# Kernel optimization log

Hardware: AMD Instinct MI355X
Metric: run time of the kernel (lower is better)

Reference implementation:

```python
import jax, jax.numpy as jnp
import numpy as np

B, S, N, F, E, EF, H, L = 4, 16, 2048, 32, 16384, 8, 64, 2
H2 = H // 2


def setup_inputs() -> dict:
    key = jax.random.key(0)
    ks = iter(jax.random.split(key, 40))

    def g(shape, s=0.05):
        return jax.random.normal(next(ks), shape, jnp.float32) * s

    return dict(
        x=jax.random.normal(next(ks), (B, S, N, F), jnp.float32),
        edge_index=jax.random.randint(next(ks), (2, E), 0, N, dtype=jnp.int32),
        edge_attr=jax.random.normal(next(ks), (E, EF), jnp.float32),
        Wp=g((F, H)), bp=jnp.zeros((H,), jnp.float32),
        Wl=g((L, H, H)), bl=jnp.zeros((L, H), jnp.float32),
        Wr=g((L, H, H)), br=jnp.zeros((L, H), jnp.float32),
        We=g((L, EF, H)), att=g((L, H)), gb=jnp.zeros((L, H), jnp.float32),
        Wih=g((L, 3 * H, H)), Whh=g((L, 3 * H, H)),
        bih=jnp.zeros((L, 3 * H), jnp.float32), bhh=jnp.zeros((L, 3 * H), jnp.float32),
        oW1=g((H, H2)), ob1=jnp.zeros((H2,), jnp.float32),
        oW2=g((H2, 1)), ob2=jnp.zeros((1,), jnp.float32),
        dW1=g((H, H2)), db1=jnp.zeros((H2,), jnp.float32),
        dW2=g((H2, 1)), db2=jnp.zeros((1,), jnp.float32),
    )


def reference(x, edge_index, edge_attr, Wp, bp, Wl, bl, Wr, br, We, att, gb,
              Wih, Whh, bih, bhh, oW1, ob1, oW2, ob2, dW1, db1, dW2, db2):
    b, s, n, f = x.shape
    nl, _, h = Wl.shape
    src, dst = edge_index[0], edge_index[1]
    # GATv2Conv add_self_loops with fill_value='mean': self-loop attr = mean of
    # incoming edge attrs per destination node (0 if none).
    ones = jnp.ones((src.shape[0],), x.dtype)
    cnt = jax.ops.segment_sum(ones, dst, num_segments=n)
    loop_attr = jax.ops.segment_sum(edge_attr, dst, num_segments=n) / jnp.maximum(cnt, 1.0)[:, None]
    ar = jnp.arange(n, dtype=src.dtype)
    src_f = jnp.concatenate([src, ar])
    dst_f = jnp.concatenate([dst, ar])
    ea_f = jnp.concatenate([edge_attr, loop_attr], axis=0)  # [E2, EF]

    def gat(Xg, l):
        # Xg: [G, N, H] -- GATv2 (heads=1) applied independently per graph.
        XL = Xg @ Wl[l] + bl[l]
        XR = Xg @ Wr[l] + br[l]
        ep = ea_f @ We[l]                              # [E2, H]
        m = XL[:, src_f] + XR[:, dst_f] + ep[None]     # [G, E2, H]
        m = jax.nn.leaky_relu(m, 0.2)
        logits = m @ att[l]                            # [G, E2]
        seg_max = jax.vmap(lambda lg: jax.ops.segment_max(lg, dst_f, num_segments=n))(logits)
        p = jnp.exp(logits - seg_max[:, dst_f])
        den = jax.vmap(lambda pg: jax.ops.segment_sum(pg, dst_f, num_segments=n))(p)
        alpha = p / den[:, dst_f]
        out = jax.vmap(lambda a, xl: jax.ops.segment_sum(a[:, None] * xl[src_f], dst_f, num_segments=n))(alpha, XL)
        return out + gb[l]

    def gru(seq, l):
        # seq: [T, M, H]; PyTorch GRU gate order (r, z, n), scan over T.
        def step(hprev, xt):
            gi = xt @ Wih[l].T + bih[l]
            gh = hprev @ Whh[l].T + bhh[l]
            ir, iz, inn = jnp.split(gi, 3, -1)
            hr, hz, hn = jnp.split(gh, 3, -1)
            r = jax.nn.sigmoid(ir + hr)
            z = jax.nn.sigmoid(iz + hz)
            nn_ = jnp.tanh(inn + r * hn)
            hnew = (1.0 - z) * nn_ + z * hprev
            return hnew, hnew
        h0 = jnp.zeros(seq.shape[1:], seq.dtype)
        _, ys = jax.lax.scan(step, h0, seq)
        return ys

    X = x @ Wp + bp  # [B, S, N, H]
    for l in range(nl):
        # Original code applies GAT per (outer-t, inner-b) pair; the inner
        # TemporalGNN's GRU recurs over the BATCH axis (length B) per outer t.
        hg = gat(X.reshape(b * s, n, h), l).reshape(b, s, n, h)
        X = gru(hg.reshape(b, s * n, h), l).reshape(b, s, n, h)
    xl = X[:, -1].reshape(b * n, h)  # x[:, -1] then per-node heads, concat dim=1
    order = jax.nn.relu(xl @ oW1 + ob1) @ oW2 + ob2
    demand = jax.nn.relu(xl @ dW1 + db1) @ dW2 + db2
    return order[None], demand[None]  # each [1, B*N, 1]
```

## Files before the change

kernel.cpp:

```cpp
#include <hip/hip_runtime.h>
#include <math.h>

#define Bb   4
#define Ss   16
#define Nn   2048
#define Ff   32
#define Ee   16384
#define EFf  8
#define Hh   64
#define HB2  32
#define E2c  (Ee + Nn)
#define RTOT (Bb*Ss*Nn)
#define Mm   (Ss*Nn)
#define CST  68

typedef __attribute__((ext_vector_type(8))) short short8;
typedef __attribute__((ext_vector_type(4))) float f32x4;
#define MFMA16 __builtin_amdgcn_mfma_f32_16x16x32_bf16

__device__ __forceinline__ float sigf(float x) { return 1.f / (1.f + __expf(-x)); }
__device__ __forceinline__ float tanhfast(float x) { return 2.f / (1.f + __expf(-2.f * x)) - 1.f; }

__device__ __forceinline__ void split_bf16(float x, unsigned short& h, unsigned short& l) {
  unsigned u = __float_as_uint(x);
  unsigned r = (u + 0x7FFFu + ((u >> 16) & 1u)) >> 16;
  h = (unsigned short)r;
  float rest = x - __uint_as_float(r << 16);
  unsigned u2 = __float_as_uint(rest);
  l = (unsigned short)((u2 + 0x7FFFu + ((u2 >> 16) & 1u)) >> 16);
}

template <int PAT>
__device__ __forceinline__ float xorf(float v) {
  return __int_as_float(__builtin_amdgcn_ds_swizzle(__float_as_int(v), PAT));
}
__device__ __forceinline__ float red8(float v) {
  int x = __builtin_amdgcn_update_dpp(0, __float_as_int(v), 0x128, 0xF, 0xF, true);
  v += __int_as_float(x);
  v += xorf<0x401F>(v);
  v += __shfl_xor(v, 32, 64);
  return v;
}
__device__ __forceinline__ float redlogit(float v) {
  int x;
  x = __builtin_amdgcn_update_dpp(0, __float_as_int(v), 0xB1, 0xF, 0xF, true);
  v += __int_as_float(x);
  x = __builtin_amdgcn_update_dpp(0, __float_as_int(v), 0x4E, 0xF, 0xF, true);
  v += __int_as_float(x);
  v += xorf<0x101F>(v);
  return v;
}

__global__ __launch_bounds__(256) void k_loop_accum(
    const int* __restrict__ ei, const float* __restrict__ ea,
    float* __restrict__ cntF, float* __restrict__ loopA) {
  int idx = blockIdx.x * 256 + threadIdx.x;
  int e = idx >> 3, j = idx & 7;
  int d = ei[Ee + e];
  atomicAdd(&loopA[d * EFf + j], ea[idx]);
  if (j == 0) atomicAdd(&cntF[d], 1.0f);
}

__global__ __launch_bounds__(256) void k_scan(
    const float* __restrict__ cntF, int* __restrict__ offs) {
  __shared__ int partial[256];
  int tid = threadIdx.x;
  int base = tid * 8;
  int vals[8];
  int s = 0;
  for (int i = 0; i < 8; ++i) {
    int c = (int)cntF[base + i] + 1;
    vals[i] = c;
    s += c;
  }
  partial[tid] = s;
  __syncthreads();
  for (int off = 1; off < 256; off <<= 1) {
    int v = partial[tid];
    int add = (tid >= off) ? partial[tid - off] : 0;
    __syncthreads();
    partial[tid] = v + add;
    __syncthreads();
  }
  int run = (tid == 0) ? 0 : partial[tid - 1];
  for (int i = 0; i < 8; ++i) {
    offs[base + i] = run;
    run += vals[i];
  }
  if (tid == 255) offs[Nn] = run;
}

__global__ __launch_bounds__(256) void k_scatter(
    const int* __restrict__ ei, const int* __restrict__ offs,
    int* __restrict__ fillI, int* __restrict__ posOf, int* __restrict__ srcA) {
  int e = blockIdx.x * 256 + threadIdx.x;
  if (e >= E2c) return;
  int d = (e < Ee) ? ei[Ee + e] : (e - Ee);
  int s = (e < Ee) ? ei[e]      : (e - Ee);
  int pos = offs[d] + atomicAdd(&fillI[d], 1);
  posOf[e] = pos;
  srcA[pos] = s;
}

__global__ __launch_bounds__(256) void k_wprep(
    const float* __restrict__ Wl, const float* __restrict__ Wr,
    const float* __restrict__ Wih, const float* __restrict__ Whh,
    unsigned short* __restrict__ WXhi, unsigned short* __restrict__ WXlo,
    unsigned short* __restrict__ WGhi, unsigned short* __restrict__ WGlo) {
  int idx = blockIdx.x * 256 + threadIdx.x;
  if (idx < 16384) {
    int j = idx & 7, lane = (idx >> 3) & 63, kh = (idx >> 9) & 1;
    int t = (idx >> 10) & 7, l = idx >> 13;
    int n = t * 16 + (lane & 15);
    int k = kh * 32 + ((lane >> 4) << 3) + j;
    const float* W = (n < 64) ? (Wl + (size_t)l * 4096) : (Wr + (size_t)l * 4096);
    float v = W[k * 64 + (n & 63)];
    unsigned short h, lo;
    split_bf16(v, h, lo);
    WXhi[idx] = h; WXlo[idx] = lo;
  } else {
    int i2 = idx - 16384;
    int j = i2 & 7, lane = (i2 >> 3) & 63, kh = (i2 >> 9) & 1;
    int t = (i2 >> 10) % 24, l = i2 / 24576;
    int n = t * 16 + (lane & 15);
    int k = kh * 32 + ((lane >> 4) << 3) + j;
    int g = n >> 6, c = n & 63;
    const float* W = (g < 3) ? (Wih + (size_t)l * 12288 + (size_t)(g * 64 + c) * 64)
                             : (Whh + (size_t)l * 12288 + (size_t)((g - 3) * 64 + c) * 64);
    float v = W[k];
    unsigned short h, lo;
    split_bf16(v, h, lo);
    WGhi[i2] = h; WGlo[i2] = lo;
  }
}

__global__ __launch_bounds__(256) void k_ep(
    const float* __restrict__ ea, const float* __restrict__ loopA,
    const float* __restrict__ We, const int* __restrict__ posOf,
    const float* __restrict__ cntF, float* __restrict__ EPc) {
  __shared__ float wlds[EFf * Hh];
  int tid = threadIdx.x;
  int l = blockIdx.y;
  const float* Wel = We + (size_t)l * EFf * Hh;
  if (tid < EFf * Hh) wlds[tid] = Wel[tid];
  if (tid + 256 < EFf * Hh) wlds[tid + 256] = Wel[tid + 256];
  __syncthreads();
  int idx = blockIdx.x * 256 + tid;
  int e = idx >> 6, j = idx & 63;
  const float* a = (e < Ee) ? (ea + (size_t)e * EFf) : (loopA + (size_t)(e - Ee) * EFf);
  float acc = 0.f;
#pragma unroll
  for (int k = 0; k < EFf; ++k) acc += a[k] * wlds[k * Hh + j];
  if (e >= Ee) acc /= fmaxf(cntF[e - Ee], 1.0f);
  EPc[(size_t)l * E2c * Hh + (((size_t)posOf[e]) << 6) + j] = acc;
}

__global__ __launch_bounds__(256) void k_proj(
    const float* __restrict__ X, const float* __restrict__ Wp,
    const float* __restrict__ bp, float* __restrict__ Out) {
  __shared__ float w[32 * 16];
  int tid = threadIdx.x;
  int j0 = blockIdx.y << 4;
  for (int idx = tid; idx < 32 * 16; idx += 256)
    w[idx] = Wp[((idx >> 4) << 6) + j0 + (idx & 15)];
  __syncthreads();
  int r0 = (blockIdx.x << 9) + tid;
  float acc[2][16];
#pragma unroll
  for (int jj = 0; jj < 16; ++jj) { float b = bp[j0 + jj]; acc[0][jj] = b; acc[1][jj] = b; }
  const float* x0 = X + ((size_t)r0 << 5);
  const float* x1 = x0 + (256 << 5);
  for (int kc = 0; kc < 8; ++kc) {
    float4 a0 = *(const float4*)(x0 + 4 * kc);
    float4 a1 = *(const float4*)(x1 + 4 * kc);
    float a0a[4] = {a0.x, a0.y, a0.z, a0.w};
    float a1a[4] = {a1.x, a1.y, a1.z, a1.w};
#pragma unroll
    for (int q = 0; q < 4; ++q) {
      const float4* wp4 = (const float4*)(w + ((4 * kc + q) << 4));
#pragma unroll
      for (int q4 = 0; q4 < 4; ++q4) {
        float4 wv = wp4[q4];
        acc[0][4*q4+0] = fmaf(a0a[q], wv.x, acc[0][4*q4+0]);
        acc[0][4*q4+1] = fmaf(a0a[q], wv.y, acc[0][4*q4+1]);
        acc[0][4*q4+2] = fmaf(a0a[q], wv.z, acc[0][4*q4+2]);
        acc[0][4*q4+3] = fmaf(a0a[q], wv.w, acc[0][4*q4+3]);
        acc[1][4*q4+0] = fmaf(a1a[q], wv.x, acc[1][4*q4+0]);
        acc[1][4*q4+1] = fmaf(a1a[q], wv.y, acc[1][4*q4+1]);
        acc[1][4*q4+2] = fmaf(a1a[q], wv.z, acc[1][4*q4+2]);
        acc[1][4*q4+3] = fmaf(a1a[q], wv.w, acc[1][4*q4+3]);
      }
    }
  }
#pragma unroll
  for (int rr = 0; rr < 2; ++rr) {
    float* op = Out + (((size_t)(r0 + 256 * rr)) << 6) + j0;
#pragma unroll
    for (int q4 = 0; q4 < 4; ++q4)
      *(float4*)(op + 4 * q4) = make_float4(acc[rr][4*q4], acc[rr][4*q4+1], acc[rr][4*q4+2], acc[rr][4*q4+3]);
  }
}

__global__ __launch_bounds__(256) void k_xlr_mm(
    const float* __restrict__ X,
    const unsigned short* __restrict__ WXhi, const unsigned short* __restrict__ WXlo,
    const float* __restrict__ bl_, const float* __restrict__ br_,
    float* __restrict__ XL, float* __restrict__ XR) {
  __shared__ unsigned short ahi[4096], alo[4096];
  __shared__ float cbuf[64 * CST];
  int tid = threadIdx.x, lane = tid & 63, wv = tid >> 6;
  size_t m0 = (size_t)blockIdx.x << 6;
#pragma unroll
  for (int it = 0; it < 2; ++it) {
    int task = (it << 8) + tid;
    int row = task >> 3, cOct = task & 7;
    const float* src = X + ((m0 + row) << 6) + (cOct << 3);
    float4 a = *(const float4*)src;
    float4 b = *(const float4*)(src + 4);
    float va[8] = {a.x, a.y, a.z, a.w, b.x, b.y, b.z, b.w};
    short8 hv, lv;
#pragma unroll
    for (int j = 0; j < 8; ++j) {
      unsigned short hs, ls;
      split_bf16(va[j], hs, ls);
      hv[j] = (short)hs; lv[j] = (short)ls;
    }
    int f = ((cOct >> 2) * 4 + (row >> 4)) * 64 + ((cOct & 3) << 4) + (row & 15);
    *(short8*)&ahi[f << 3] = hv;
    *(short8*)&alo[f << 3] = lv;
  }
  __syncthreads();
  short8 Ah0 = *(const short8*)&ahi[((0 + wv) << 6 | lane) << 3];
  short8 Al0 = *(const short8*)&alo[((0 + wv) << 6 | lane) << 3];
  short8 Ah1 = *(const short8*)&ahi[((4 + wv) << 6 | lane) << 3];
  short8 Al1 = *(const short8*)&alo[((4 + wv) << 6 | lane) << 3];
  int nl = lane & 15;
  f32x4 acc[8];
#pragma unroll
  for (int t = 0; t < 8; ++t) {
    int n = t * 16 + nl;
    float b = (n < 64) ? bl_[n] : br_[n - 64];
    acc[t] = (f32x4){b, b, b, b};
  }
#pragma unroll
  for (int t = 0; t < 8; ++t) {
    const short8* bh0p = (const short8*)(WXhi + ((t << 1) << 9)) + lane;
    const short8* bl0p = (const short8*)(WXlo + ((t << 1) << 9)) + lane;
    const short8* bh1p = (const short8*)(WXhi + (((t << 1) + 1) << 9)) + lane;
    const short8* bl1p = (const short8*)(WXlo + (((t << 1) + 1) << 9)) + lane;
    short8 bh0 = *bh0p, bl0 = *bl0p, bh1 = *bh1p, bl1 = *bl1p;
    acc[t] = MFMA16(Ah0, bh0, acc[t], 0, 0, 0);
    acc[t] = MFMA16(Ah0, bl0, acc[t], 0, 0, 0);
    acc[t] = MFMA16(Al0, bh0, acc[t], 0, 0, 0);
    acc[t] = MFMA16(Ah1, bh1, acc[t], 0, 0, 0);
    acc[t] = MFMA16(Ah1, bl1, acc[t], 0, 0, 0);
    acc[t] = MFMA16(Al1, bh1, acc[t], 0, 0, 0);
  }
  int rbase = (wv << 4) + ((lane >> 4) << 2);
#pragma unroll
  for (int half = 0; half < 2; ++half) {
    __syncthreads();
#pragma unroll
    for (int tt = 0; tt < 4; ++tt) {
      int t = (half << 2) + tt;
#pragma unroll
      for (int reg = 0; reg < 4; ++reg)
        cbuf[(rbase + reg) * CST + (tt << 4) + nl] = acc[t][reg];
    }
    __syncthreads();
    float* dst = half ? XR : XL;
#pragma unroll
    for (int i = 0; i < 4; ++i) {
      int idx = (i << 10) + (tid << 2);
      int row = idx >> 6, col = idx & 63;
      *(float4*)(dst + ((m0 + row) << 6) + col) = *(float4*)&cbuf[row * CST + col];
    }
  }
}

__global__ __launch_bounds__(256) void k_gat(
    const float* __restrict__ XL, float* __restrict__ XR_HG,
    const float* __restrict__ EPc, const int* __restrict__ offs,
    const int* __restrict__ srcA,
    const float* __restrict__ att, const float* __restrict__ gbl) {
  int d = blockIdx.x;
  int q = blockIdx.y;
  int tid = threadIdx.x;
  int wv = tid >> 6, lane = tid & 63;
  int eSub = lane >> 3, hOct = lane & 7;
  int hb = hOct << 3;
  float at[8], gv[8];
  {
    float4 a0 = *(const float4*)(att + hb);
    float4 a1 = *(const float4*)(att + hb + 4);
    float4 g0v = *(const float4*)(gbl + hb);
    float4 g1v = *(const float4*)(gbl + hb + 4);
    at[0]=a0.x; at[1]=a0.y; at[2]=a0.z; at[3]=a0.w;
    at[4]=a1.x; at[5]=a1.y; at[6]=a1.z; at[7]=a1.w;
    gv[0]=g0v.x; gv[1]=g0v.y; gv[2]=g0v.z; gv[3]=g0v.w;
    gv[4]=g1v.x; gv[5]=g1v.y; gv[6]=g1v.z; gv[7]=g1v.w;
  }
  int p0 = offs[d], p1 = offs[d + 1];
  int nE = p1 - p0;
  int nCh = (nE + 7) >> 3;
  int g0 = (q << 3) + wv;
  int g1 = g0 + 4;
  size_t rowA = ((size_t)(g0 * Nn + d)) << 6;
  size_t rowB = ((size_t)(g1 * Nn + d)) << 6;
  float xrA[8], xrB[8];
  {
    float4 a = *(const float4*)(XR_HG + rowA + hb);
    float4 b = *(const float4*)(XR_HG + rowA + hb + 4);
    float4 c = *(const float4*)(XR_HG + rowB + hb);
    float4 e = *(const float4*)(XR_HG + rowB + hb + 4);
    xrA[0]=a.x; xrA[1]=a.y; xrA[2]=a.z; xrA[3]=a.w; xrA[4]=b.x; xrA[5]=b.y; xrA[6]=b.z; xrA[7]=b.w;
    xrB[0]=c.x; xrB[1]=c.y; xrB[2]=c.z; xrB[3]=c.w; xrB[4]=e.x; xrB[5]=e.y; xrB[6]=e.z; xrB[7]=e.w;
  }
  const float* XA = XL + (((size_t)g0 * Nn) << 6);
  const float* XB = XL + (((size_t)g1 * Nn) << 6);
  float SsA = 0.f, SsB = 0.f;
  float accA[8], accB[8];
#pragma unroll
  for (int j = 0; j < 8; ++j) { accA[j] = 0.f; accB[j] = 0.f; }
  for (int c = 0; c < nCh; ++c) {
    int p = (c << 3) + eSub;
    int pc = p < nE ? p : nE - 1;
    int s = srcA[p0 + pc];
    const float* epp = EPc + (((size_t)(p0 + pc)) << 6) + hb;
    float4 e0 = *(const float4*)epp;
    float4 e1 = *(const float4*)(epp + 4);
    float ep[8] = {e0.x, e0.y, e0.z, e0.w, e1.x, e1.y, e1.z, e1.w};
    const float* xap = XA + ((size_t)s << 6) + hb;
    const float* xbp = XB + ((size_t)s << 6) + hb;
    float4 xa0 = *(const float4*)xap, xa1 = *(const float4*)(xap + 4);
    float4 xb0 = *(const float4*)xbp, xb1 = *(const float4*)(xbp + 4);
    float xA[8] = {xa0.x, xa0.y, xa0.z, xa0.w, xa1.x, xa1.y, xa1.z, xa1.w};
    float xB[8] = {xb0.x, xb0.y, xb0.z, xb0.w, xb1.x, xb1.y, xb1.z, xb1.w};
    float vA = 0.f, vB = 0.f;
#pragma unroll
    for (int j = 0; j < 8; ++j) {
      float mA = xA[j] + xrA[j] + ep[j];
      mA = fmaxf(mA, 0.2f * mA);
      vA = fmaf(mA, at[j], vA);
      float mB = xB[j] + xrB[j] + ep[j];
      mB = fmaxf(mB, 0.2f * mB);
      vB = fmaf(mB, at[j], vB);
    }
    vA = redlogit(vA);
    vB = redlogit(vB);
    float wA = (p < nE) ? __expf(vA) : 0.f;
    float wB = (p < nE) ? __expf(vB) : 0.f;
    SsA += wA; SsB += wB;
#pragma unroll
    for (int j = 0; j < 8; ++j) {
      accA[j] = fmaf(wA, xA[j], accA[j]);
      accB[j] = fmaf(wB, xB[j], accB[j]);
    }
  }
  SsA = red8(SsA); SsB = red8(SsB);
#pragma unroll
  for (int j = 0; j < 8; ++j) { accA[j] = red8(accA[j]); accB[j] = red8(accB[j]); }
  if (eSub == 0) {
    float invA = 1.f / SsA, invB = 1.f / SsB;
    float* opA = XR_HG + rowA + hb;
    float* opB = XR_HG + rowB + hb;
    *(float4*)(opA)     = make_float4(fmaf(accA[0], invA, gv[0]), fmaf(accA[1], invA, gv[1]),
                                      fmaf(accA[2], invA, gv[2]), fmaf(accA[3], invA, gv[3]));
    *(float4*)(opA + 4) = make_float4(fmaf(accA[4], invA, gv[4]), fmaf(accA[5], invA, gv[5]),
                                      fmaf(accA[6], invA, gv[6]), fmaf(accA[7], invA, gv[7]));
    *(float4*)(opB)     = make_float4(fmaf(accB[0], invB, gv[0]), fmaf(accB[1], invB, gv[1]),
                                      fmaf(accB[2], invB, gv[2]), fmaf(accB[3], invB, gv[3]));
    *(float4*)(opB + 4) = make_float4(fmaf(accB[4], invB, gv[4]), fmaf(accB[5], invB, gv[5]),
                                      fmaf(accB[6], invB, gv[6]), fmaf(accB[7], invB, gv[7]));
  }
}

template <int HASP>
__global__ __launch_bounds__(256) void k_gru_mm(
    const float* __restrict__ hg, const float* __restrict__ hp,
    const unsigned short* __restrict__ WGhi, const unsigned short* __restrict__ WGlo,
    const float* __restrict__ bih, const float* __restrict__ bhh,
    float* __restrict__ hout) {
  __shared__ unsigned short ghi[4096], glo[4096], phi[4096], plo[4096];
  __shared__ float cbuf[64 * CST];
  int tid = threadIdx.x, lane = tid & 63, wv = tid >> 6;
  size_t m0 = (size_t)blockIdx.x << 6;
#pragma unroll
  for (int it = 0; it < 2; ++it) {
    int task = (it << 8) + tid;
    int row = task >> 3, cOct = task & 7;
    const float* srcg = hg + ((m0 + row) << 6) + (cOct << 3);
    float4 a = *(const float4*)srcg;
    float4 b = *(const float4*)(srcg + 4);
    float va[8] = {a.x, a.y, a.z, a.w, b.x, b.y, b.z, b.w};
    short8 hv, lv;
#pragma unroll
    for (int j = 0; j < 8; ++j) {
      unsigned short hs, ls;
      split_bf16(va[j], hs, ls);
      hv[j] = (short)hs; lv[j] = (short)ls;
    }
    int f = ((cOct >> 2) * 4 + (row >> 4)) * 64 + ((cOct & 3) << 4) + (row & 15);
    *(short8*)&ghi[f << 3] = hv;
    *(short8*)&glo[f << 3] = lv;
    if (HASP) {
      const float* srcp = hp + ((m0 + row) << 6) + (cOct << 3);
      float4 c = *(const float4*)srcp;
      float4 e = *(const float4*)(srcp + 4);
      float vp[8] = {c.x, c.y, c.z, c.w, e.x, e.y, e.z, e.w};
#pragma unroll
      for (int j = 0; j < 8; ++j) {
        unsigned short hs, ls;
        split_bf16(vp[j], hs, ls);
        hv[j] = (short)hs; lv[j] = (short)ls;
      }
      *(short8*)&phi[f << 3] = hv;
      *(short8*)&plo[f << 3] = lv;
    }
  }
  __syncthreads();
  short8 Gh0 = *(const short8*)&ghi[((0 + wv) << 6 | lane) << 3];
  short8 Gl0 = *(const short8*)&glo[((0 + wv) << 6 | lane) << 3];
  short8 Gh1 = *(const short8*)&ghi[((4 + wv) << 6 | lane) << 3];
  short8 Gl1 = *(const short8*)&glo[((4 + wv) << 6 | lane) << 3];
  short8 Ph0, Pl0, Ph1, Pl1;
  if (HASP) {
    Ph0 = *(const short8*)&phi[((0 + wv) << 6 | lane) << 3];
    Pl0 = *(const short8*)&plo[((0 + wv) << 6 | lane) << 3];
    Ph1 = *(const short8*)&phi[((4 + wv) << 6 | lane) << 3];
    Pl1 = *(const short8*)&plo[((4 + wv) << 6 | lane) << 3];
  }
  int nl = lane & 15;
  f32x4 acc[24];
#pragma unroll
  for (int t = 0; t < 24; ++t) {
    int g = t >> 2;
    int c = ((t & 3) << 4) + nl;
    float b = (g < 3) ? bih[(g << 6) + c] : bhh[((g - 3) << 6) + c];
    acc[t] = (f32x4){b, b, b, b};
  }
#pragma unroll
  for (int t = 0; t < 12; ++t) {
    const short8* bh0p = (const short8*)(WGhi + ((t << 1) << 9)) + lane;
    const short8* bl0p = (const short8*)(WGlo + ((t << 1) << 9)) + lane;
    const short8* bh1p = (const short8*)(WGhi + (((t << 1) + 1) << 9)) + lane;
    const short8* bl1p = (const short8*)(WGlo + (((t << 1) + 1) << 9)) + lane;
    short8 bh0 = *bh0p, bl0 = *bl0p, bh1 = *bh1p, bl1 = *bl1p;
    acc[t] = MFMA16(Gh0, bh0, acc[t], 0, 0, 0);
    acc[t] = MFMA16(Gh0, bl0, acc[t], 0, 0, 0);
    acc[t] = MFMA16(Gl0, bh0, acc[t], 0, 0, 0);
    acc[t] = MFMA16(Gh1, bh1, acc[t], 0, 0, 0);
    acc[t] = MFMA16(Gh1, bl1, acc[t], 0, 0, 0);
    acc[t] = MFMA16(Gl1, bh1, acc[t], 0, 0, 0);
  }
  if (HASP) {
#pragma unroll
    for (int t = 12; t < 24; ++t) {
      const short8* bh0p = (const short8*)(WGhi + ((t << 1) << 9)) + lane;
      const short8* bl0p = (const short8*)(WGlo + ((t << 1) << 9)) + lane;
      const short8* bh1p = (const short8*)(WGhi + (((t << 1) + 1) << 9)) + lane;
      const short8* bl1p = (const short8*)(WGlo + (((t << 1) + 1) << 9)) + lane;
      short8 bh0 = *bh0p, bl0 = *bl0p, bh1 = *bh1p, bl1 = *bl1p;
      acc[t] = MFMA16(Ph0, bh0, acc[t], 0, 0, 0);
      acc[t] = MFMA16(Ph0, bl0, acc[t], 0, 0, 0);
      acc[t] = MFMA16(Pl0, bh0, acc[t], 0, 0, 0);
      acc[t] = MFMA16(Ph1, bh1, acc[t], 0, 0, 0);
      acc[t] = MFMA16(Ph1, bl1, acc[t], 0, 0, 0);
      acc[t] = MFMA16(Pl1, bh1, acc[t], 0, 0, 0);
    }
  }
  int rbase = (wv << 4) + ((lane >> 4) << 2);
#pragma unroll
  for (int ct = 0; ct < 4; ++ct) {
    int c = (ct << 4) + nl;
#pragma unroll
    for (int reg = 0; reg < 4; ++reg) {
      size_t rowg = m0 + rbase + reg;
      float rg = sigf(acc[ct][reg]      + acc[12 + ct][reg]);
      float zg = sigf(acc[4 + ct][reg]  + acc[16 + ct][reg]);
      float ng = tanhfast(acc[8 + ct][reg] + rg * acc[20 + ct][reg]);
      float hv = HASP ? hp[(rowg << 6) + c] : 0.f;
      cbuf[(rbase + reg) * CST + c] = (1.f - zg) * ng + zg * hv;
    }
  }
  __syncthreads();
#pragma unroll
  for (int i = 0; i < 4; ++i) {
    int idx = (i << 10) + (tid << 2);
    int row = idx >> 6, col = idx & 63;
    *(float4*)(hout + ((m0 + row) << 6) + col) = *(float4*)&cbuf[row * CST + col];
  }
}

__global__ __launch_bounds__(256) void k_heads(
    const float* __restrict__ Xb,
    const float* __restrict__ oW1, const float* __restrict__ ob1,
    const float* __restrict__ oW2, const float* __restrict__ ob2,
    const float* __restrict__ dW1, const float* __restrict__ db1,
    const float* __restrict__ dW2, const float* __restrict__ db2,
    float* __restrict__ out) {
  __shared__ float xa[64 * 65];
  __shared__ float w1o[64 * 32], w1d[64 * 32];
  __shared__ float po[4][64], pd[4][64];
  int tid = threadIdx.x;
  int rblk = blockIdx.x << 6;
  int b = rblk >> 11;
  int n0 = rblk & (Nn - 1);
  const float* src = Xb + (((size_t)b * Ss + (Ss - 1)) * Nn + n0) * Hh;
#pragma unroll
  for (int i = 0; i < 4; ++i) {
    int idx = (i << 10) + (tid << 2);
    int row = idx >> 6, col = idx & 63;
    float4 v = *(const float4*)(src + idx);
    float* dp = &xa[row * 65 + col];
    dp[0] = v.x; dp[1] = v.y; dp[2] = v.z; dp[3] = v.w;
  }
  for (int idx = tid; idx < 2048; idx += 256) {
    w1o[idx] = oW1[idx];
    w1d[idx] = dW1[idx];
  }
  __syncthreads();
  int row = tid & 63;
  int jg = tid >> 6;
  int j0 = jg << 3;
  float hO[8], hD[8];
#pragma unroll
  for (int j = 0; j < 8; ++j) { hO[j] = ob1[j0 + j]; hD[j] = db1[j0 + j]; }
  const float* xr = &xa[row * 65];
  for (int k = 0; k < 64; ++k) {
    float xv = xr[k];
    const float4* wo = (const float4*)&w1o[(k << 5) + j0];
    const float4* wd = (const float4*)&w1d[(k << 5) + j0];
    float4 o0 = wo[0], o1 = wo[1], d0 = wd[0], d1 = wd[1];
    hO[0] = fmaf(xv, o0.x, hO[0]); hO[1] = fmaf(xv, o0.y, hO[1]);
    hO[2] = fmaf(xv, o0.z, hO[2]); hO[3] = fmaf(xv, o0.w, hO[3]);
    hO[4] = fmaf(xv, o1.x, hO[4]); hO[5] = fmaf(xv, o1.y, hO[5]);
    hO[6] = fmaf(xv, o1.z, hO[6]); hO[7] = fmaf(xv, o1.w, hO[7]);
    hD[0] = fmaf(xv, d0.x, hD[0]); hD[1] = fmaf(xv, d0.y, hD[1]);
    hD[2] = fmaf(xv, d0.z, hD[2]); hD[3] = fmaf(xv, d0.w, hD[3]);
    hD[4] = fmaf(xv, d1.x, hD[4]); hD[5] = fmaf(xv, d1.y, hD[5]);
    hD[6] = fmaf(xv, d1.z, hD[6]); hD[7] = fmaf(xv, d1.w, hD[7]);
  }
  float accoP = 0.f, accdP = 0.f;
#pragma unroll
  for (int j = 0; j < 8; ++j) {
    accoP = fmaf(fmaxf(hO[j], 0.f), oW2[j0 + j], accoP);
    accdP = fmaf(fmaxf(hD[j], 0.f), dW2[j0 + j], accdP);
  }
  po[jg][row] = accoP;
  pd[jg][row] = accdP;
  __syncthreads();
  if (tid < 64) {
    int r = rblk + tid;
    out[r]           = ob2[0] + ((po[0][tid] + po[1][tid]) + (po[2][tid] + po[3][tid]));
    out[Bb * Nn + r] = db2[0] + ((pd[0][tid] + pd[1][tid]) + (pd[2][tid] + pd[3][tid]));
  }
}

extern "C" void kernel_launch(void* const* d_in, const int* in_sizes, int n_in,
                              void* d_out, int out_size, void* d_ws, size_t ws_size,
                              hipStream_t stream) {
  const float* x   = (const float*)d_in[0];
  const int*   ei  = (const int*)d_in[1];
  const float* ea  = (const float*)d_in[2];
  const float* Wp  = (const float*)d_in[3];
  const float* bp  = (const float*)d_in[4];
  const float* Wl  = (const float*)d_in[5];
  const float* bl  = (const float*)d_in[6];
  const float* Wr  = (const float*)d_in[7];
  const float* br  = (const float*)d_in[8];
  const float* We  = (const float*)d_in[9];
  const float* att = (const float*)d_in[10];
  const float* gb  = (const float*)d_in[11];
  const float* Wih = (const float*)d_in[12];
  const float* Whh = (const float*)d_in[13];
  const float* bih = (const float*)d_in[14];
  const float* bhh = (const float*)d_in[15];
  const float* oW1 = (const float*)d_in[16];
  const float* ob1 = (const float*)d_in[17];
  const float* oW2 = (const float*)d_in[18];
  const float* ob2 = (const float*)d_in[19];
  const float* dW1 = (const float*)d_in[20];
  const float* db1 = (const float*)d_in[21];
  const float* dW2 = (const float*)d_in[22];
  const float* db2 = (const float*)d_in[23];
  float* out = (float*)d_out;

  float* f    = (float*)d_ws;
  float* Xb   = f;
  float* XLb  = Xb  + (size_t)RTOT * Hh;
  float* XRb  = XLb + (size_t)RTOT * Hh;
  float* EPc  = XRb + (size_t)RTOT * Hh;
  unsigned short* WXhi = (unsigned short*)(EPc + (size_t)2 * E2c * Hh);
  unsigned short* WXlo = WXhi + 16384;
  unsigned short* WGhi = WXlo + 16384;
  unsigned short* WGlo = WGhi + 49152;
  float* cntF = (float*)(WGlo + 49152);
  float* loopA = cntF + Nn;
  int*   fillI = (int*)(loopA + Nn * EFf);
  int*   offs  = fillI + Nn;
  int*   posOf = offs + 2052;
  int*   srcA  = posOf + E2c;

  hipMemsetAsync(cntF, 0, (size_t)(Nn + Nn * EFf + Nn) * 4, stream);

  k_loop_accum<<<dim3(Ee * EFf / 256), 256, 0, stream>>>(ei, ea, cntF, loopA);
  k_scan<<<1, 256, 0, stream>>>(cntF, offs);
  k_scatter<<<dim3((E2c + 255) / 256), 256, 0, stream>>>(ei, offs, fillI, posOf, srcA);
  k_wprep<<<dim3(256), 256, 0, stream>>>(Wl, Wr, Wih, Whh, WXhi, WXlo, WGhi, WGlo);

  k_proj<<<dim3(RTOT / 512, 4), 256, 0, stream>>>(x, Wp, bp, Xb);

  k_ep<<<dim3(E2c * Hh / 256, 2), 256, 0, stream>>>(ea, loopA, We, posOf, cntF, EPc);

  for (int l = 0; l < 2; ++l) {
    k_xlr_mm<<<dim3(RTOT / 64), 256, 0, stream>>>(
        Xb, WXhi + (size_t)l * 8192, WXlo + (size_t)l * 8192,
        bl + (size_t)l * Hh, br + (size_t)l * Hh, XLb, XRb);
    k_gat<<<dim3(Nn, 8), 256, 0, stream>>>(
        XLb, XRb, EPc + (size_t)l * E2c * Hh, offs, srcA,
        att + (size_t)l * Hh, gb + (size_t)l * Hh);
    const unsigned short* WGh_l = WGhi + (size_t)l * 24576;
    const unsigned short* WGl_l = WGlo + (size_t)l * 24576;
    const float* bih_l = bih + (size_t)l * 192;
    const float* bhh_l = bhh + (size_t)l * 192;
    for (int t = 0; t < Bb; ++t) {
      const float* hg_t = XRb + (size_t)t * Mm * Hh;
      float* h_out = Xb + (size_t)t * Mm * Hh;
      if (t == 0) {
        k_gru_mm<0><<<dim3(Mm / 64), 256, 0, stream>>>(
            hg_t, nullptr, WGh_l, WGl_l, bih_l, bhh_l, h_out);
      } else {
        const float* h_prev = Xb + (size_t)(t - 1) * Mm * Hh;
        k_gru_mm<1><<<dim3(Mm / 64), 256, 0, stream>>>(
            hg_t, h_prev, WGh_l, WGl_l, bih_l, bhh_l, h_out);
      }
    }
  }

  k_heads<<<dim3(Bb * Nn / 64), 256, 0, stream>>>(
      Xb, oW1, ob1, oW2, ob2, dW1, db1, dW2, db2, out);
}
```

Before: 425.0 us.

## Split GRU matmul kernel across two column halves via blockIdx.y

The GRU step kernel now launches a second grid dimension, and each block computes only 32 of the 64 hidden output columns for its 64 rows. This halves the accumulator registers per thread (12 f32x4 instead of 24), which should raise occupancy and double the number of blocks. In exchange, both column-half blocks redo the bf16 hi/lo split and LDS staging of the full input and previous-state tiles, so those loads and conversions happen twice.

```diff
diff --git a/kernel.cpp b/kernel.cpp
--- a/kernel.cpp
+++ b/kernel.cpp
@@ -13,6 +13,7 @@
 #define RTOT (Bb*Ss*Nn)
 #define Mm   (Ss*Nn)
 #define CST  68
+#define GST  36
 
 typedef __attribute__((ext_vector_type(8))) short short8;
 typedef __attribute__((ext_vector_type(4))) float f32x4;
@@ -382,8 +383,9 @@
     const float* __restrict__ bih, const float* __restrict__ bhh,
     float* __restrict__ hout) {
   __shared__ unsigned short ghi[4096], glo[4096], phi[4096], plo[4096];
-  __shared__ float cbuf[64 * CST];
+  __shared__ float cbuf[64 * GST];
   int tid = threadIdx.x, lane = tid & 63, wv = tid >> 6;
+  int ch = blockIdx.y;
   size_t m0 = (size_t)blockIdx.x << 6;
 #pragma unroll
   for (int it = 0; it < 2; ++it) {
@@ -431,64 +433,74 @@
     Pl1 = *(const short8*)&plo[((4 + wv) << 6 | lane) << 3];
   }
   int nl = lane & 15;
-  f32x4 acc[24];
-#pragma unroll
-  for (int t = 0; t < 24; ++t) {
-    int g = t >> 2;
-    int c = ((t & 3) << 4) + nl;
-    float b = (g < 3) ? bih[(g << 6) + c] : bhh[((g - 3) << 6) + c];
-    acc[t] = (f32x4){b, b, b, b};
-  }
-#pragma unroll
-  for (int t = 0; t < 12; ++t) {
-    const short8* bh0p = (const short8*)(WGhi + ((t << 1) << 9)) + lane;
-    const short8* bl0p = (const short8*)(WGlo + ((t << 1) << 9)) + lane;
-    const short8* bh1p = (const short8*)(WGhi + (((t << 1) + 1) << 9)) + lane;
-    const short8* bl1p = (const short8*)(WGlo + (((t << 1) + 1) << 9)) + lane;
-    short8 bh0 = *bh0p, bl0 = *bl0p, bh1 = *bh1p, bl1 = *bl1p;
-    acc[t] = MFMA16(Gh0, bh0, acc[t], 0, 0, 0);
-    acc[t] = MFMA16(Gh0, bl0, acc[t], 0, 0, 0);
-    acc[t] = MFMA16(Gl0, bh0, acc[t], 0, 0, 0);
-    acc[t] = MFMA16(Gh1, bh1, acc[t], 0, 0, 0);
-    acc[t] = MFMA16(Gh1, bl1, acc[t], 0, 0, 0);
-    acc[t] = MFMA16(Gl1, bh1, acc[t], 0, 0, 0);
-  }
-  if (HASP) {
-#pragma unroll
-    for (int t = 12; t < 24; ++t) {
+  f32x4 acc[12];
+#pragma unroll
+  for (int g = 0; g < 6; ++g)
+#pragma unroll
+    for (int ct2 = 0; ct2 < 2; ++ct2) {
+      int c = (((ch << 1) + ct2) << 4) + nl;
+      float b = (g < 3) ? bih[(g << 6) + c] : bhh[((g - 3) << 6) + c];
+      acc[(g << 1) + ct2] = (f32x4){b, b, b, b};
+    }
+#pragma unroll
+  for (int g = 0; g < 3; ++g)
+#pragma unroll
+    for (int ct2 = 0; ct2 < 2; ++ct2) {
+      int t = (g << 2) + (ch << 1) + ct2;
       const short8* bh0p = (const short8*)(WGhi + ((t << 1) << 9)) + lane;
       const short8* bl0p = (const short8*)(WGlo + ((t << 1) << 9)) + lane;
       const short8* bh1p = (const short8*)(WGhi + (((t << 1) + 1) << 9)) + lane;
       const short8* bl1p = (const short8*)(WGlo + (((t << 1) + 1) << 9)) + lane;
       short8 bh0 = *bh0p, bl0 = *bl0p, bh1 = *bh1p, bl1 = *bl1p;
-      acc[t] = MFMA16(Ph0, bh0, acc[t], 0, 0, 0);
-      acc[t] = MFMA16(Ph0, bl0, acc[t], 0, 0, 0);
-      acc[t] = MFMA16(Pl0, bh0, acc[t], 0, 0, 0);
-      acc[t] = MFMA16(Ph1, bh1, acc[t], 0, 0, 0);
-      acc[t] = MFMA16(Ph1, bl1, acc[t], 0, 0, 0);
-      acc[t] = MFMA16(Pl1, bh1, acc[t], 0, 0, 0);
-    }
+      int a = (g << 1) + ct2;
+      acc[a] = MFMA16(Gh0, bh0, acc[a], 0, 0, 0);
+      acc[a] = MFMA16(Gh0, bl0, acc[a], 0, 0, 0);
+      acc[a] = MFMA16(Gl0, bh0, acc[a], 0, 0, 0);
+      acc[a] = MFMA16(Gh1, bh1, acc[a], 0, 0, 0);
+      acc[a] = MFMA16(Gh1, bl1, acc[a], 0, 0, 0);
+      acc[a] = MFMA16(Gl1, bh1, acc[a], 0, 0, 0);
+    }
+  if (HASP) {
+#pragma unroll
+    for (int g = 0; g < 3; ++g)
+#pragma unroll
+      for (int ct2 = 0; ct2 < 2; ++ct2) {
+        int t = 12 + (g << 2) + (ch << 1) + ct2;
+        const short8* bh0p = (const short8*)(WGhi + ((t << 1) << 9)) + lane;
+        const short8* bl0p = (const short8*)(WGlo + ((t << 1) << 9)) + lane;
+        const short8* bh1p = (const short8*)(WGhi + (((t << 1) + 1) << 9)) + lane;
+        const short8* bl1p = (const short8*)(WGlo + (((t << 1) + 1) << 9)) + lane;
+        short8 bh0 = *bh0p, bl0 = *bl0p, bh1 = *bh1p, bl1 = *bl1p;
+        int a = 6 + (g << 1) + ct2;
+        acc[a] = MFMA16(Ph0, bh0, acc[a], 0, 0, 0);
+        acc[a] = MFMA16(Ph0, bl0, acc[a], 0, 0, 0);
+        acc[a] = MFMA16(Pl0, bh0, acc[a], 0, 0, 0);
+        acc[a] = MFMA16(Ph1, bh1, acc[a], 0, 0, 0);
+        acc[a] = MFMA16(Ph1, bl1, acc[a], 0, 0, 0);
+        acc[a] = MFMA16(Pl1, bh1, acc[a], 0, 0, 0);
+      }
   }
   int rbase = (wv << 4) + ((lane >> 4) << 2);
 #pragma unroll
-  for (int ct = 0; ct < 4; ++ct) {
-    int c = (ct << 4) + nl;
+  for (int ct2 = 0; ct2 < 2; ++ct2) {
+    int c = (((ch << 1) + ct2) << 4) + nl;
+    int cl = (ct2 << 4) + nl;
 #pragma unroll
     for (int reg = 0; reg < 4; ++reg) {
       size_t rowg = m0 + rbase + reg;
-      float rg = sigf(acc[ct][reg]      + acc[12 + ct][reg]);
-      float zg = sigf(acc[4 + ct][reg]  + acc[16 + ct][reg]);
-      float ng = tanhfast(acc[8 + ct][reg] + rg * acc[20 + ct][reg]);
+      float rg = sigf(acc[ct2][reg]      + acc[6 + ct2][reg]);
+      float zg = sigf(acc[2 + ct2][reg]  + acc[8 + ct2][reg]);
+      float ng = tanhfast(acc[4 + ct2][reg] + rg * acc[10 + ct2][reg]);
       float hv = HASP ? hp[(rowg << 6) + c] : 0.f;
-      cbuf[(rbase + reg) * CST + c] = (1.f - zg) * ng + zg * hv;
-    }
-  }
-  __syncthreads();
-#pragma unroll
-  for (int i = 0; i < 4; ++i) {
+      cbuf[(rbase + reg) * GST + cl] = (1.f - zg) * ng + zg * hv;
+    }
+  }
+  __syncthreads();
+#pragma unroll
+  for (int i = 0; i < 2; ++i) {
     int idx = (i << 10) + (tid << 2);
-    int row = idx >> 6, col = idx & 63;
-    *(float4*)(hout + ((m0 + row) << 6) + col) = *(float4*)&cbuf[row * CST + col];
+    int row = idx >> 5, col = idx & 31;
+    *(float4*)(hout + ((m0 + row) << 6) + (ch << 5) + col) = *(float4*)&cbuf[row * GST + col];
   }
 }
 
@@ -628,11 +640,11 @@
       const float* hg_t = XRb + (size_t)t * Mm * Hh;
       float* h_out = Xb + (size_t)t * Mm * Hh;
       if (t == 0) {
-        k_gru_mm<0><<<dim3(Mm / 64), 256, 0, stream>>>(
+        k_gru_mm<0><<<dim3(Mm / 64, 2), 256, 0, stream>>>(
             hg_t, nullptr, WGh_l, WGl_l, bih_l, bhh_l, h_out);
       } else {
         const float* h_prev = Xb + (size_t)(t - 1) * Mm * Hh;
-        k_gru_mm<1><<<dim3(Mm / 64), 256, 0, stream>>>(
+        k_gru_mm<1><<<dim3(Mm / 64, 2), 256, 0, stream>>>(
             hg_t, h_prev, WGh_l, WGl_l, bih_l, bhh_l, h_out);
       }
     }
```

Result: no change. 422.0 us (-0.7%).
